# Kernel tuning notes

Hardware: AMD Instinct MI355X
Metric: run time of the kernel (lower is better)

Reference implementation:

```python
import jax, jax.numpy as jnp
import numpy as np

L, D, H, FF = 6, 768, 12, 3072
DH = D // H
EPS = 1e-12

def _layer_norm(x, g, b):
    mu = jnp.mean(x, axis=-1, keepdims=True)
    var = jnp.mean((x - mu) ** 2, axis=-1, keepdims=True)
    return (x - mu) * jax.lax.rsqrt(var + EPS) * g + b

def setup_inputs() -> dict:
    key = jax.random.key(0)
    ks = jax.random.split(key, 12)
    s = 0.02
    inp = {
        "x": jax.random.normal(ks[0], (8, 512, D), dtype=jnp.float32),
        "attn_mask": jnp.ones((8, 512), dtype=jnp.int32),
        "Wq": jax.random.normal(ks[1], (L, D, D), dtype=jnp.float32) * s,
        "bq": jnp.zeros((L, D), dtype=jnp.float32),
        "Wk": jax.random.normal(ks[2], (L, D, D), dtype=jnp.float32) * s,
        "bk": jnp.zeros((L, D), dtype=jnp.float32),
        "Wv": jax.random.normal(ks[3], (L, D, D), dtype=jnp.float32) * s,
        "bv": jnp.zeros((L, D), dtype=jnp.float32),
        "Wo": jax.random.normal(ks[4], (L, D, D), dtype=jnp.float32) * s,
        "bo": jnp.zeros((L, D), dtype=jnp.float32),
        "ln1_g": jnp.ones((L, D), dtype=jnp.float32),
        "ln1_b": jnp.zeros((L, D), dtype=jnp.float32),
        "W1": jax.random.normal(ks[5], (L, D, FF), dtype=jnp.float32) * s,
        "b1": jnp.zeros((L, FF), dtype=jnp.float32),
        "W2": jax.random.normal(ks[6], (L, FF, D), dtype=jnp.float32) * s,
        "b2": jnp.zeros((L, D), dtype=jnp.float32),
        "ln2_g": jnp.ones((L, D), dtype=jnp.float32),
        "ln2_b": jnp.zeros((L, D), dtype=jnp.float32),
    }
    return inp

def reference(x, attn_mask, Wq, bq, Wk, bk, Wv, bv, Wo, bo,
              ln1_g, ln1_b, W1, b1, W2, b2, ln2_g, ln2_b):
    bs, S, _ = x.shape
    mask_neg = (attn_mask == 0)[:, None, None, :]  # (bs,1,1,S)
    h = x
    for i in range(L):
        def split_heads(t):
            return t.reshape(bs, S, H, DH).transpose(0, 2, 1, 3)  # (bs,H,S,dh)
        q = split_heads(h @ Wq[i] + bq[i]) / jnp.sqrt(jnp.float32(DH))
        k = split_heads(h @ Wk[i] + bk[i])
        v = split_heads(h @ Wv[i] + bv[i])
        scores = jnp.einsum('bhqd,bhkd->bhqk', q, k)
        scores = jnp.where(mask_neg, jnp.float32(-1e9), scores)
        w = jax.nn.softmax(scores, axis=-1)
        ctx = jnp.einsum('bhqk,bhkd->bhqd', w, v)
        ctx = ctx.transpose(0, 2, 1, 3).reshape(bs, S, D)
        sa = ctx @ Wo[i] + bo[i]
        h2 = _layer_norm(sa + h, ln1_g[i], ln1_b[i])
        ffn = jax.nn.gelu(h2 @ W1[i] + b1[i], approximate=False) @ W2[i] + b2[i]
        h = _layer_norm(ffn + h2, ln2_g[i], ln2_b[i])
    return h
```

## Files before the change

kernel.cpp:

```cpp
#include <hip/hip_runtime.h>
#include <math.h>

#define NLAYER 6
#define DMODEL 768
#define NHEAD 12
#define DHEAD 64
#define FFDIM 3072
#define SEQ 512
#define BATCH 8
#define NTOK (BATCH * SEQ)
#define ND ((size_t)NTOK * DMODEL)

typedef __bf16 bf16_t;
typedef __bf16 bf16x8 __attribute__((ext_vector_type(8)));
typedef float f32x4 __attribute__((ext_vector_type(4)));

__device__ __forceinline__ float bf2f(ushort u) {
    return __uint_as_float(((unsigned int)u) << 16);
}
union BFU { __bf16 h; ushort u; };
__device__ __forceinline__ ushort f2b(float x) { BFU c; c.h = (__bf16)x; return c.u; }

#define GLDS(gp, lp) __builtin_amdgcn_global_load_lds( \
    (const __attribute__((address_space(1))) void*)(gp), \
    (__attribute__((address_space(3))) void*)(lp), 16, 0, 0)

__global__ __launch_bounds__(256) void gemm_mfma(
    const ushort* __restrict__ A, const ushort* __restrict__ Bt,
    const float* __restrict__ bias, float* __restrict__ Cf,
    ushort* __restrict__ Cb, int M, int K, int N, int act)
{
    __shared__ __align__(16) ushort As[8192];
    __shared__ __align__(16) ushort Bs[8192];

    const int t = threadIdx.x;
    const int w = t >> 6, l = t & 63;
    const int wr = w >> 1, wc = w & 1;
    const int row0 = blockIdx.y * 128, col0 = blockIdx.x * 128;

    f32x4 acc[4][4];
#pragma unroll
    for (int mi = 0; mi < 4; ++mi)
#pragma unroll
        for (int ni = 0; ni < 4; ++ni)
#pragma unroll
            for (int e = 0; e < 4; ++e) acc[mi][ni][e] = 0.f;

    const int c0 = t,       r0 = c0 >> 2, kg0 = (c0 & 3) ^ ((r0 >> 1) & 3);
    const int c1 = t + 256, r1 = c1 >> 2, kg1 = (c1 & 3) ^ ((r1 >> 1) & 3);
    const ushort* gA0 = A + (size_t)(row0 + r0) * K + kg0 * 8;
    const ushort* gA1 = A + (size_t)(row0 + r1) * K + kg1 * 8;
    const ushort* gB0 = Bt + (size_t)(col0 + r0) * K + kg0 * 8;
    const ushort* gB1 = Bt + (size_t)(col0 + r1) * K + kg1 * 8;

    const int lm = l & 15, lq = l >> 4;
    int aoff[4], boff[4];
#pragma unroll
    for (int mi = 0; mi < 4; ++mi) {
        int m = wr * 64 + mi * 16 + lm;
        aoff[mi] = m * 32 + (lq ^ ((m >> 1) & 3)) * 8;
    }
#pragma unroll
    for (int ni = 0; ni < 4; ++ni) {
        int n = wc * 64 + ni * 16 + lm;
        boff[ni] = n * 32 + (lq ^ ((n >> 1) & 3)) * 8;
    }

#define STAGE_FF(b, k0) do {                                  \
        GLDS(gA0 + (k0), &As[(b) * 4096 + w * 512]);          \
        GLDS(gA1 + (k0), &As[(b) * 4096 + 2048 + w * 512]);   \
        GLDS(gB0 + (k0), &Bs[(b) * 4096 + w * 512]);          \
        GLDS(gB1 + (k0), &Bs[(b) * 4096 + 2048 + w * 512]);   \
    } while (0)

#define COMPUTE_FF(b) do {                                                  \
        bf16x8 af[4], bfr[4];                                               \
        _Pragma("unroll")                                                   \
        for (int mi = 0; mi < 4; ++mi)                                      \
            af[mi] = *(const bf16x8*)&As[(b) * 4096 + aoff[mi]];            \
        _Pragma("unroll")                                                   \
        for (int ni = 0; ni < 4; ++ni)                                      \
            bfr[ni] = *(const bf16x8*)&Bs[(b) * 4096 + boff[ni]];           \
        _Pragma("unroll")                                                   \
        for (int mi = 0; mi < 4; ++mi)                                      \
            _Pragma("unroll")                                               \
            for (int ni = 0; ni < 4; ++ni)                                  \
                acc[mi][ni] = __builtin_amdgcn_mfma_f32_16x16x32_bf16(      \
                    af[mi], bfr[ni], acc[mi][ni], 0, 0, 0);                 \
    } while (0)

    const int nsteps = K >> 5;
    STAGE_FF(0, 0);
    __syncthreads();
    int cur = 0;
    for (int s = 0; s < nsteps - 1; ++s) {
        STAGE_FF(cur ^ 1, (s + 1) * 32);
        COMPUTE_FF(cur);
        __syncthreads();
        cur ^= 1;
    }
    COMPUTE_FF(cur);

#pragma unroll
    for (int mi = 0; mi < 4; ++mi) {
        int rowb = row0 + wr * 64 + mi * 16 + lq * 4;
#pragma unroll
        for (int ni = 0; ni < 4; ++ni) {
            int col = col0 + wc * 64 + ni * 16 + lm;
            float bv = bias[col];
#pragma unroll
            for (int r = 0; r < 4; ++r) {
                float v = acc[mi][ni][r] + bv;
                if (act == 1) v = 0.5f * v * (1.0f + erff(v * 0.70710678118654752f));
                size_t idx = (size_t)(rowb + r) * N + col;
                if (Cb) ((bf16_t*)Cb)[idx] = (bf16_t)v;
                else    Cf[idx] = v;
            }
        }
    }
#undef STAGE_FF
#undef COMPUTE_FF
}

__global__ __launch_bounds__(256) void gemm_mfma_sk(
    const ushort* __restrict__ A, const ushort* __restrict__ Bt,
    const float* __restrict__ bias, float* __restrict__ P0,
    float* __restrict__ P1, int M, int K, int N, int kLen)
{
    __shared__ __align__(16) ushort As[4096];
    __shared__ __align__(16) ushort Bs[8192];

    const int t = threadIdx.x;
    const int w = t >> 6, l = t & 63;
    const int wr = w >> 1, wc = w & 1;
    const int row0 = blockIdx.y * 64, col0 = blockIdx.x * 128;
    const int z = blockIdx.z;
    const int kOff = z * kLen;
    float* Pz = (z == 0) ? P0 : P1;

    f32x4 acc[2][4];
#pragma unroll
    for (int mi = 0; mi < 2; ++mi)
#pragma unroll
        for (int ni = 0; ni < 4; ++ni)
#pragma unroll
            for (int e = 0; e < 4; ++e) acc[mi][ni][e] = 0.f;

    const int rS = t >> 2, kg = (t & 3) ^ ((rS >> 1) & 3);
    const ushort* gA  = A  + (size_t)(row0 + rS) * K + kg * 8;
    const ushort* gB0 = Bt + (size_t)(col0 + rS) * K + kg * 8;
    const ushort* gB1 = Bt + (size_t)(col0 + 64 + rS) * K + kg * 8;

    const int lm = l & 15, lq = l >> 4;
    int aoff[2], boff[4];
#pragma unroll
    for (int mi = 0; mi < 2; ++mi) {
        int m = wr * 32 + mi * 16 + lm;
        aoff[mi] = m * 32 + (lq ^ ((m >> 1) & 3)) * 8;
    }
#pragma unroll
    for (int ni = 0; ni < 4; ++ni) {
        int n = wc * 64 + ni * 16 + lm;
        boff[ni] = n * 32 + (lq ^ ((n >> 1) & 3)) * 8;
    }

#define STAGE_SK(b, k0) do {                                  \
        GLDS(gA  + (k0), &As[(b) * 2048 + w * 512]);          \
        GLDS(gB0 + (k0), &Bs[(b) * 4096 + w * 512]);          \
        GLDS(gB1 + (k0), &Bs[(b) * 4096 + 2048 + w * 512]);   \
    } while (0)

#define COMPUTE_SK(b) do {                                                  \
        bf16x8 af[2], bfr[4];                                               \
        _Pragma("unroll")                                                   \
        for (int mi = 0; mi < 2; ++mi)                                      \
            af[mi] = *(const bf16x8*)&As[(b) * 2048 + aoff[mi]];            \
        _Pragma("unroll")                                                   \
        for (int ni = 0; ni < 4; ++ni)                                      \
            bfr[ni] = *(const bf16x8*)&Bs[(b) * 4096 + boff[ni]];           \
        _Pragma("unroll")                                                   \
        for (int mi = 0; mi < 2; ++mi)                                      \
            _Pragma("unroll")                                               \
            for (int ni = 0; ni < 4; ++ni)                                  \
                acc[mi][ni] = __builtin_amdgcn_mfma_f32_16x16x32_bf16(      \
                    af[mi], bfr[ni], acc[mi][ni], 0, 0, 0);                 \
    } while (0)

    const int nsteps = kLen >> 5;
    STAGE_SK(0, kOff);
    __syncthreads();
    int cur = 0;
    for (int s = 0; s < nsteps - 1; ++s) {
        STAGE_SK(cur ^ 1, kOff + (s + 1) * 32);
        COMPUTE_SK(cur);
        __syncthreads();
        cur ^= 1;
    }
    COMPUTE_SK(cur);

#pragma unroll
    for (int mi = 0; mi < 2; ++mi) {
        int rowb = row0 + wr * 32 + mi * 16 + lq * 4;
#pragma unroll
        for (int ni = 0; ni < 4; ++ni) {
            int col = col0 + wc * 64 + ni * 16 + lm;
            float bv = (z == 0) ? bias[col] : 0.f;
#pragma unroll
            for (int r = 0; r < 4; ++r)
                Pz[(size_t)(rowb + r) * N + col] = acc[mi][ni][r] + bv;
        }
    }
#undef STAGE_SK
#undef COMPUTE_SK
}

__global__ __launch_bounds__(256) void gemm_qkv(
    const ushort* __restrict__ A, const ushort* __restrict__ Bt,
    const float* __restrict__ bq, const float* __restrict__ bk,
    const float* __restrict__ bv,
    ushort* __restrict__ qb, ushort* __restrict__ kb, ushort* __restrict__ vtb)
{
    __shared__ __align__(16) ushort As[4096];
    __shared__ __align__(16) ushort Bs[8192];

    const int K = DMODEL;
    const int t = threadIdx.x;
    const int w = t >> 6, l = t & 63;
    const int wr = w >> 1, wc = w & 1;
    const int row0 = blockIdx.y * 64, col0 = blockIdx.x * 128;
    const int seg = blockIdx.x / 6;

    f32x4 acc[2][4];
#pragma unroll
    for (int mi = 0; mi < 2; ++mi)
#pragma unroll
        for (int ni = 0; ni < 4; ++ni)
#pragma unroll
            for (int e = 0; e < 4; ++e) acc[mi][ni][e] = 0.f;

    const int rS = t >> 2, kg = (t & 3) ^ ((rS >> 1) & 3);
    const ushort* gA  = A  + (size_t)(row0 + rS) * K + kg * 8;
    const ushort* gB0 = Bt + (size_t)(col0 + rS) * K + kg * 8;
    const ushort* gB1 = Bt + (size_t)(col0 + 64 + rS) * K + kg * 8;

    const int lm = l & 15, lq = l >> 4;
    int aoff[2], boff[4];
#pragma unroll
    for (int mi = 0; mi < 2; ++mi) {
        int m = wr * 32 + mi * 16 + lm;
        aoff[mi] = m * 32 + (lq ^ ((m >> 1) & 3)) * 8;
    }
#pragma unroll
    for (int ni = 0; ni < 4; ++ni) {
        int n = wc * 64 + ni * 16 + lm;
        boff[ni] = n * 32 + (lq ^ ((n >> 1) & 3)) * 8;
    }

#define STAGE_QKV(b, k0) do {                                 \
        GLDS(gA  + (k0), &As[(b) * 2048 + w * 512]);          \
        GLDS(gB0 + (k0), &Bs[(b) * 4096 + w * 512]);          \
        GLDS(gB1 + (k0), &Bs[(b) * 4096 + 2048 + w * 512]);   \
    } while (0)

#define COMPUTE_QKV(b) do {                                                 \
        bf16x8 af[2], bfr[4];                                               \
        _Pragma("unroll")                                                   \
        for (int mi = 0; mi < 2; ++mi)                                      \
            af[mi] = *(const bf16x8*)&As[(b) * 2048 + aoff[mi]];            \
        _Pragma("unroll")                                                   \
        for (int ni = 0; ni < 4; ++ni)                                      \
            bfr[ni] = *(const bf16x8*)&Bs[(b) * 4096 + boff[ni]];           \
        _Pragma("unroll")                                                   \
        for (int mi = 0; mi < 2; ++mi)                                      \
            _Pragma("unroll")                                               \
            for (int ni = 0; ni < 4; ++ni)                                  \
                acc[mi][ni] = __builtin_amdgcn_mfma_f32_16x16x32_bf16(      \
                    af[mi], bfr[ni], acc[mi][ni], 0, 0, 0);                 \
    } while (0)

    const int nsteps = K >> 5;
    STAGE_QKV(0, 0);
    __syncthreads();
    int cur = 0;
    for (int s = 0; s < nsteps - 1; ++s) {
        STAGE_QKV(cur ^ 1, (s + 1) * 32);
        COMPUTE_QKV(cur);
        __syncthreads();
        cur ^= 1;
    }
    COMPUTE_QKV(cur);

    const float* bp = (seg == 0) ? bq : (seg == 1) ? bk : bv;
    const float sc = (seg == 0) ? 0.125f : 1.0f;
#pragma unroll
    for (int mi = 0; mi < 2; ++mi) {
        int rowb = row0 + wr * 32 + mi * 16 + lq * 4;
#pragma unroll
        for (int ni = 0; ni < 4; ++ni) {
            int col = col0 + wc * 64 + ni * 16 + lm;
            int lcol = col - seg * 768;
            float bvv = bp[lcol];
            if (seg == 2) {
                int hh = lcol >> 6, dd = lcol & 63;
                int bb = rowb >> 9, ss = rowb & 511;
                ushort4 o;
                o.x = f2b(acc[mi][ni][0] + bvv);
                o.y = f2b(acc[mi][ni][1] + bvv);
                o.z = f2b(acc[mi][ni][2] + bvv);
                o.w = f2b(acc[mi][ni][3] + bvv);
                *(ushort4*)&vtb[(((size_t)(bb * NHEAD + hh)) * DHEAD + dd) * SEQ + ss] = o;
            } else {
                ushort* dst = seg ? kb : qb;
#pragma unroll
                for (int r = 0; r < 4; ++r)
                    dst[(size_t)(rowb + r) * DMODEL + lcol] = f2b((acc[mi][ni][r] + bvv) * sc);
            }
        }
    }
#undef STAGE_QKV
#undef COMPUTE_QKV
}

#define QSTR 72

__global__ __launch_bounds__(256) void attn_mfma(
    const ushort* __restrict__ qb, const ushort* __restrict__ kb,
    const ushort* __restrict__ vtb, const int* __restrict__ mask,
    ushort* __restrict__ ctxb)
{
    __shared__ __align__(16) ushort Qs[64 * QSTR];
    __shared__ __align__(16) ushort Ks[64 * QSTR];
    __shared__ __align__(16) ushort Vs[64 * QSTR];
    __shared__ __align__(16) ushort Ps[64 * QSTR];
    __shared__ float Ma[64];

    const int qt = blockIdx.x, h = blockIdx.y, b = blockIdx.z;
    const int t = threadIdx.x;
    const int w = t >> 6, l = t & 63;
    const int lm = l & 15, lq = l >> 4;

#pragma unroll
    for (int i = 0; i < 2; ++i) {
        int ch = t + i * 256;
        int r = ch >> 3, c8 = ch & 7;
        *(uint4*)&Qs[r * QSTR + c8 * 8] =
            *(const uint4*)&qb[((size_t)(b * SEQ + qt * 64 + r)) * DMODEL + h * DHEAD + c8 * 8];
    }

    f32x4 O[4];
#pragma unroll
    for (int n0 = 0; n0 < 4; ++n0)
#pragma unroll
        for (int e = 0; e < 4; ++e) O[n0][e] = 0.f;
    float mrow[4] = {-3.4e38f, -3.4e38f, -3.4e38f, -3.4e38f};
    float lrow[4] = {0.f, 0.f, 0.f, 0.f};

    const int qrow = w * 16 + lm;
    const int prow = w * 16 + lq * 4;

    for (int kt = 0; kt < SEQ / 64; ++kt) {
#pragma unroll
        for (int i = 0; i < 2; ++i) {
            int ch = t + i * 256;
            int r = ch >> 3, c8 = ch & 7;
            *(uint4*)&Ks[r * QSTR + c8 * 8] =
                *(const uint4*)&kb[((size_t)(b * SEQ + kt * 64 + r)) * DMODEL + h * DHEAD + c8 * 8];
            *(uint4*)&Vs[r * QSTR + c8 * 8] =
                *(const uint4*)&vtb[(((size_t)(b * NHEAD + h)) * DHEAD + r) * SEQ + kt * 64 + c8 * 8];
        }
        if (t < 64) Ma[t] = (mask[b * SEQ + kt * 64 + t] == 0) ? -1e9f : 0.f;
        __syncthreads();

        bf16x8 aq0 = *(const bf16x8*)&Qs[qrow * QSTR + lq * 8];
        bf16x8 aq1 = *(const bf16x8*)&Qs[qrow * QSTR + lq * 8 + 32];
        f32x4 S[4];
#pragma unroll
        for (int n0 = 0; n0 < 4; ++n0) {
#pragma unroll
            for (int e = 0; e < 4; ++e) S[n0][e] = 0.f;
            bf16x8 b0 = *(const bf16x8*)&Ks[(n0 * 16 + lm) * QSTR + lq * 8];
            bf16x8 b1 = *(const bf16x8*)&Ks[(n0 * 16 + lm) * QSTR + lq * 8 + 32];
            S[n0] = __builtin_amdgcn_mfma_f32_16x16x32_bf16(aq0, b0, S[n0], 0, 0, 0);
            S[n0] = __builtin_amdgcn_mfma_f32_16x16x32_bf16(aq1, b1, S[n0], 0, 0, 0);
        }

        float ma4[4];
#pragma unroll
        for (int n0 = 0; n0 < 4; ++n0) ma4[n0] = Ma[n0 * 16 + lm];
#pragma unroll
        for (int n0 = 0; n0 < 4; ++n0)
#pragma unroll
            for (int r = 0; r < 4; ++r) S[n0][r] += ma4[n0];

        float tm[4];
#pragma unroll
        for (int r = 0; r < 4; ++r)
            tm[r] = fmaxf(fmaxf(S[0][r], S[1][r]), fmaxf(S[2][r], S[3][r]));
#pragma unroll
        for (int off = 1; off < 16; off <<= 1)
#pragma unroll
            for (int r = 0; r < 4; ++r)
                tm[r] = fmaxf(tm[r], __shfl_xor(tm[r], off, 64));

        float al[4], ts[4];
#pragma unroll
        for (int r = 0; r < 4; ++r) {
            float mn = fmaxf(mrow[r], tm[r]);
            al[r] = __expf(mrow[r] - mn);
            mrow[r] = mn;
            ts[r] = 0.f;
        }
#pragma unroll
        for (int n0 = 0; n0 < 4; ++n0)
#pragma unroll
            for (int r = 0; r < 4; ++r) {
                float p = __expf(S[n0][r] - mrow[r]);
                ts[r] += p;
                Ps[(prow + r) * QSTR + n0 * 16 + lm] = f2b(p);
            }
#pragma unroll
        for (int off = 1; off < 16; off <<= 1)
#pragma unroll
            for (int r = 0; r < 4; ++r)
                ts[r] += __shfl_xor(ts[r], off, 64);
#pragma unroll
        for (int r = 0; r < 4; ++r) lrow[r] = lrow[r] * al[r] + ts[r];
#pragma unroll
        for (int n0 = 0; n0 < 4; ++n0)
#pragma unroll
            for (int r = 0; r < 4; ++r) O[n0][r] *= al[r];

        bf16x8 ap0 = *(const bf16x8*)&Ps[qrow * QSTR + lq * 8];
        bf16x8 ap1 = *(const bf16x8*)&Ps[qrow * QSTR + lq * 8 + 32];
#pragma unroll
        for (int n0 = 0; n0 < 4; ++n0) {
            bf16x8 v0 = *(const bf16x8*)&Vs[(n0 * 16 + lm) * QSTR + lq * 8];
            bf16x8 v1 = *(const bf16x8*)&Vs[(n0 * 16 + lm) * QSTR + lq * 8 + 32];
            O[n0] = __builtin_amdgcn_mfma_f32_16x16x32_bf16(ap0, v0, O[n0], 0, 0, 0);
            O[n0] = __builtin_amdgcn_mfma_f32_16x16x32_bf16(ap1, v1, O[n0], 0, 0, 0);
        }
        __syncthreads();
    }

    float inv[4];
#pragma unroll
    for (int r = 0; r < 4; ++r) inv[r] = 1.f / lrow[r];
#pragma unroll
    for (int n0 = 0; n0 < 4; ++n0)
#pragma unroll
        for (int r = 0; r < 4; ++r)
            Ks[(prow + r) * QSTR + n0 * 16 + lm] = f2b(O[n0][r] * inv[r]);
    __syncthreads();
#pragma unroll
    for (int i = 0; i < 2; ++i) {
        int ch = t + i * 256;
        int r = ch >> 3, c8 = ch & 7;
        *(uint4*)&ctxb[((size_t)(b * SEQ + qt * 64 + r)) * DMODEL + h * DHEAD + c8 * 8] =
            *(const uint4*)&Ks[r * QSTR + c8 * 8];
    }
}

__global__ __launch_bounds__(256) void transpose_w(
    const float* __restrict__ Wq, const float* __restrict__ Wk,
    const float* __restrict__ Wv, const float* __restrict__ Wo,
    const float* __restrict__ W1, const float* __restrict__ W2,
    ushort* __restrict__ Wqt, ushort* __restrict__ Wkt,
    ushort* __restrict__ Wvt, ushort* __restrict__ Wot,
    ushort* __restrict__ W1t, ushort* __restrict__ W2t)
{
    __shared__ float tile[32][33];
    const int bid = blockIdx.x;
    const float* src; ushort* dst; int K, N, tx, ty;
    if (bid < 2304) {
        int m = bid / 576, tl = bid % 576;
        src = (m == 0) ? Wq : (m == 1) ? Wk : (m == 2) ? Wv : Wo;
        dst = (m == 0) ? Wqt : (m == 1) ? Wkt : (m == 2) ? Wvt : Wot;
        K = 768; N = 768; tx = tl % 24; ty = tl / 24;
    } else if (bid < 4608) {
        int tl = bid - 2304;
        src = W1; dst = W1t; K = 768; N = 3072; tx = tl % 96; ty = tl / 96;
    } else {
        int tl = bid - 4608;
        src = W2; dst = W2t; K = 3072; N = 768; tx = tl % 24; ty = tl / 24;
    }
    const int t = threadIdx.x;
    const int lx = t & 31, ly = t >> 5;
    const int n0 = tx * 32, k0 = ty * 32;
#pragma unroll
    for (int i = 0; i < 4; ++i)
        tile[lx][ly + i * 8] = src[(size_t)(k0 + ly + i * 8) * N + n0 + lx];
    __syncthreads();
#pragma unroll
    for (int i = 0; i < 4; ++i)
        ((bf16_t*)dst)[(size_t)(n0 + ly + i * 8) * K + k0 + lx] =
            (bf16_t)tile[ly + i * 8][lx];
}

__global__ __launch_bounds__(256) void f2bf_kernel(
    const float* __restrict__ src, ushort* __restrict__ dst)
{
    const size_t i = ((size_t)blockIdx.x * 256 + threadIdx.x) * 4;
    float4 v = *(const float4*)(src + i);
    ushort4 o;
    o.x = f2b(v.x); o.y = f2b(v.y); o.z = f2b(v.z); o.w = f2b(v.w);
    *(ushort4*)(dst + i) = o;
}

__global__ __launch_bounds__(256) void add_ln3_kernel(
    const float* __restrict__ p0, const float* __restrict__ p1,
    const float* __restrict__ res,
    const float* __restrict__ gw, const float* __restrict__ bw,
    float* __restrict__ out, ushort* __restrict__ outb)
{
    const int row = blockIdx.x;
    const int t = threadIdx.x;
    __shared__ float red[8];

    const float* a0 = p0 + (size_t)row * DMODEL;
    const float* a1 = p1 + (size_t)row * DMODEL;
    const float* rr = res + (size_t)row * DMODEL;

    float vals[3];
    float s = 0.f;
#pragma unroll
    for (int i = 0; i < 3; ++i) {
        int c = t + i * 256;
        vals[i] = a0[c] + a1[c] + rr[c];
        s += vals[i];
    }
#pragma unroll
    for (int off = 32; off > 0; off >>= 1) s += __shfl_down(s, off, 64);
    if ((t & 63) == 0) red[t >> 6] = s;
    __syncthreads();
    const float mu = (red[0] + red[1] + red[2] + red[3]) * (1.0f / DMODEL);

    float vs = 0.f;
#pragma unroll
    for (int i = 0; i < 3; ++i) {
        float d = vals[i] - mu;
        vs += d * d;
    }
#pragma unroll
    for (int off = 32; off > 0; off >>= 1) vs += __shfl_down(vs, off, 64);
    if ((t & 63) == 0) red[4 + (t >> 6)] = vs;
    __syncthreads();
    const float var = (red[4] + red[5] + red[6] + red[7]) * (1.0f / DMODEL);
    const float inv = rsqrtf(var + 1e-12f);

#pragma unroll
    for (int i = 0; i < 3; ++i) {
        int c = t + i * 256;
        float v = (vals[i] - mu) * inv * gw[c] + bw[c];
        out[(size_t)row * DMODEL + c] = v;
        ((bf16_t*)outb)[(size_t)row * DMODEL + c] = (bf16_t)v;
    }
}

extern "C" void kernel_launch(void* const* d_in, const int* in_sizes, int n_in,
                              void* d_out, int out_size, void* d_ws, size_t ws_size,
                              hipStream_t stream)
{
    const float* x    = (const float*)d_in[0];
    const int*   mask = (const int*)d_in[1];
    const float* Wq = (const float*)d_in[2];
    const float* bq = (const float*)d_in[3];
    const float* Wk = (const float*)d_in[4];
    const float* bk = (const float*)d_in[5];
    const float* Wv = (const float*)d_in[6];
    const float* bv = (const float*)d_in[7];
    const float* Wo = (const float*)d_in[8];
    const float* bo = (const float*)d_in[9];
    const float* ln1g = (const float*)d_in[10];
    const float* ln1b = (const float*)d_in[11];
    const float* W1 = (const float*)d_in[12];
    const float* b1 = (const float*)d_in[13];
    const float* W2 = (const float*)d_in[14];
    const float* b2 = (const float*)d_in[15];
    const float* ln2g = (const float*)d_in[16];
    const float* ln2b = (const float*)d_in[17];

    float* f32b = (float*)d_ws;
    float* hbuf = f32b;
    float* f1   = f32b + ND;
    float* h2   = f32b + 2 * ND;
    ushort* ub  = (ushort*)(f32b + 3 * ND);
    ushort* qb  = ub;
    ushort* kb  = ub + ND;
    ushort* vtb = ub + 2 * ND;
    ushort* hb  = ub + 3 * ND;
    ushort* U   = ub + 4 * ND;
    ushort* ctxb = U;
    ushort* Wqkvt = U + (size_t)NTOK * FFDIM;
    ushort* Wot = Wqkvt + 3 * 768 * 768;
    ushort* W1t = Wot + 768 * 768;
    ushort* W2t = W1t + (size_t)768 * 3072;

    float* p1 = (float*)ub;

    hipMemcpyAsync(hbuf, x, ND * sizeof(float), hipMemcpyDeviceToDevice, stream);
    f2bf_kernel<<<(int)(ND / 1024), 256, 0, stream>>>(x, hb);

    const dim3 gQKV(18, 64);
    const dim3 gSK(6, 64, 2);
    const dim3 gFF(24, 32);
    const dim3 gA(SEQ / 64, NHEAD, BATCH);

    for (int l = 0; l < NLAYER; ++l) {
        const float* Wq_l = Wq + (size_t)l * DMODEL * DMODEL;
        const float* Wk_l = Wk + (size_t)l * DMODEL * DMODEL;
        const float* Wv_l = Wv + (size_t)l * DMODEL * DMODEL;
        const float* Wo_l = Wo + (size_t)l * DMODEL * DMODEL;
        const float* W1_l = W1 + (size_t)l * DMODEL * FFDIM;
        const float* W2_l = W2 + (size_t)l * FFDIM * DMODEL;

        transpose_w<<<6912, 256, 0, stream>>>(Wq_l, Wk_l, Wv_l, Wo_l, W1_l, W2_l,
                                              Wqkvt, Wqkvt + 768 * 768,
                                              Wqkvt + 2 * 768 * 768, Wot, W1t, W2t);

        gemm_qkv<<<gQKV, 256, 0, stream>>>(hb, Wqkvt,
                                           bq + (size_t)l * DMODEL,
                                           bk + (size_t)l * DMODEL,
                                           bv + (size_t)l * DMODEL,
                                           qb, kb, vtb);

        attn_mfma<<<gA, 256, 0, stream>>>(qb, kb, vtb, mask, ctxb);

        gemm_mfma_sk<<<gSK, 256, 0, stream>>>(ctxb, Wot, bo + (size_t)l * DMODEL,
                                              f1, p1, NTOK, DMODEL, DMODEL, DMODEL / 2);

        add_ln3_kernel<<<NTOK, 256, 0, stream>>>(f1, p1, hbuf,
                                                 ln1g + (size_t)l * DMODEL,
                                                 ln1b + (size_t)l * DMODEL, h2, hb);

        gemm_mfma<<<gFF, 256, 0, stream>>>(hb, W1t, b1 + (size_t)l * FFDIM,
                                           nullptr, U, NTOK, DMODEL, FFDIM, 1);

        gemm_mfma_sk<<<gSK, 256, 0, stream>>>(U, W2t, b2 + (size_t)l * DMODEL,
                                              f1, p1, NTOK, FFDIM, DMODEL, FFDIM / 2);

        float* hout = (l == NLAYER - 1) ? (float*)d_out : hbuf;
        add_ln3_kernel<<<NTOK, 256, 0, stream>>>(f1, p1, h2,
                                                 ln2g + (size_t)l * DMODEL,
                                                 ln2b + (size_t)l * DMODEL, hout, hb);
    }
}
```

Before: 1.284 ms.

## Swizzle GEMM workgroup order for XCDs, vectorize layernorm and transpose, fuse init

Remaps workgroup indices in all three GEMM kernels so consecutive blocks land on the same XCD (stride-8 interleave), aiming to improve L2 reuse of A/B tiles. Rewrites add+layernorm to use 192 threads with float4 loads and stores, writes the transpose output as paired bf16 stores, and merges the initial memcpy and bf16 conversion into one kernel. The swizzle assumes grid sizes divisible by 8 and hardcodes grid dimensions in two kernels.

Result: faster. 1.247 ms (-2.8%).

```diff
diff --git a/kernel.cpp b/kernel.cpp
--- a/kernel.cpp
+++ b/kernel.cpp
@@ -36,7 +36,13 @@
     const int t = threadIdx.x;
     const int w = t >> 6, l = t & 63;
     const int wr = w >> 1, wc = w & 1;
-    const int row0 = blockIdx.y * 128, col0 = blockIdx.x * 128;
+
+    const int hw = blockIdx.x + gridDim.x * blockIdx.y;
+    const int nwg = gridDim.x * gridDim.y;
+    const int sw = (hw & 7) * (nwg >> 3) + (hw >> 3);
+    const int bx = sw % gridDim.x, by = sw / gridDim.x;
+
+    const int row0 = by * 128, col0 = bx * 128;
 
     f32x4 acc[4][4];
 #pragma unroll
@@ -89,11 +95,11 @@
                     af[mi], bfr[ni], acc[mi][ni], 0, 0, 0);                 \
     } while (0)
 
-    const int nsteps = K >> 5;
+    const int nst = K >> 5;
     STAGE_FF(0, 0);
     __syncthreads();
     int cur = 0;
-    for (int s = 0; s < nsteps - 1; ++s) {
+    for (int s = 0; s < nst - 1; ++s) {
         STAGE_FF(cur ^ 1, (s + 1) * 32);
         COMPUTE_FF(cur);
         __syncthreads();
@@ -133,8 +139,14 @@
     const int t = threadIdx.x;
     const int w = t >> 6, l = t & 63;
     const int wr = w >> 1, wc = w & 1;
-    const int row0 = blockIdx.y * 64, col0 = blockIdx.x * 128;
-    const int z = blockIdx.z;
+
+    const int hw = blockIdx.x + 6 * blockIdx.y + 384 * blockIdx.z;
+    const int sw = (hw & 7) * 96 + (hw >> 3);
+    const int z  = sw / 384;
+    const int rr_ = sw - z * 384;
+    const int bx = rr_ % 6, by = rr_ / 6;
+
+    const int row0 = by * 64, col0 = bx * 128;
     const int kOff = z * kLen;
     float* Pz = (z == 0) ? P0 : P1;
 
@@ -186,11 +198,11 @@
                     af[mi], bfr[ni], acc[mi][ni], 0, 0, 0);                 \
     } while (0)
 
-    const int nsteps = kLen >> 5;
+    const int nst = kLen >> 5;
     STAGE_SK(0, kOff);
     __syncthreads();
     int cur = 0;
-    for (int s = 0; s < nsteps - 1; ++s) {
+    for (int s = 0; s < nst - 1; ++s) {
         STAGE_SK(cur ^ 1, kOff + (s + 1) * 32);
         COMPUTE_SK(cur);
         __syncthreads();
@@ -227,8 +239,13 @@
     const int t = threadIdx.x;
     const int w = t >> 6, l = t & 63;
     const int wr = w >> 1, wc = w & 1;
-    const int row0 = blockIdx.y * 64, col0 = blockIdx.x * 128;
-    const int seg = blockIdx.x / 6;
+
+    const int hw = blockIdx.x + 18 * blockIdx.y;
+    const int sw = (hw & 7) * 144 + (hw >> 3);
+    const int bx = sw % 18, by = sw / 18;
+
+    const int row0 = by * 64, col0 = bx * 128;
+    const int seg = bx / 6;
 
     f32x4 acc[2][4];
 #pragma unroll
@@ -278,11 +295,11 @@
                     af[mi], bfr[ni], acc[mi][ni], 0, 0, 0);                 \
     } while (0)
 
-    const int nsteps = K >> 5;
+    const int nst = K >> 5;
     STAGE_QKV(0, 0);
     __syncthreads();
     int cur = 0;
-    for (int s = 0; s < nsteps - 1; ++s) {
+    for (int s = 0; s < nst - 1; ++s) {
         STAGE_QKV(cur ^ 1, (s + 1) * 32);
         COMPUTE_QKV(cur);
         __syncthreads();
@@ -490,23 +507,30 @@
     for (int i = 0; i < 4; ++i)
         tile[lx][ly + i * 8] = src[(size_t)(k0 + ly + i * 8) * N + n0 + lx];
     __syncthreads();
-#pragma unroll
-    for (int i = 0; i < 4; ++i)
-        ((bf16_t*)dst)[(size_t)(n0 + ly + i * 8) * K + k0 + lx] =
-            (bf16_t)tile[ly + i * 8][lx];
-}
-
-__global__ __launch_bounds__(256) void f2bf_kernel(
-    const float* __restrict__ src, ushort* __restrict__ dst)
+    const int kk2 = (t & 15) * 2, nn = t >> 4;
+#pragma unroll
+    for (int i = 0; i < 2; ++i) {
+        int nl = nn + i * 16;
+        ushort2 o;
+        o.x = f2b(tile[nl][kk2]);
+        o.y = f2b(tile[nl][kk2 + 1]);
+        *(ushort2*)&dst[(size_t)(n0 + nl) * K + k0 + kk2] = o;
+    }
+}
+
+__global__ __launch_bounds__(256) void init_kernel(
+    const float* __restrict__ x, float* __restrict__ hbuf,
+    ushort* __restrict__ hb)
 {
     const size_t i = ((size_t)blockIdx.x * 256 + threadIdx.x) * 4;
-    float4 v = *(const float4*)(src + i);
+    float4 v = *(const float4*)(x + i);
+    *(float4*)(hbuf + i) = v;
     ushort4 o;
     o.x = f2b(v.x); o.y = f2b(v.y); o.z = f2b(v.z); o.w = f2b(v.w);
-    *(ushort4*)(dst + i) = o;
-}
-
-__global__ __launch_bounds__(256) void add_ln3_kernel(
+    *(ushort4*)(hb + i) = o;
+}
+
+__global__ __launch_bounds__(192) void add_ln3_kernel(
     const float* __restrict__ p0, const float* __restrict__ p1,
     const float* __restrict__ res,
     const float* __restrict__ gw, const float* __restrict__ bw,
@@ -514,46 +538,45 @@
 {
     const int row = blockIdx.x;
     const int t = threadIdx.x;
-    __shared__ float red[8];
-
-    const float* a0 = p0 + (size_t)row * DMODEL;
-    const float* a1 = p1 + (size_t)row * DMODEL;
-    const float* rr = res + (size_t)row * DMODEL;
-
-    float vals[3];
-    float s = 0.f;
-#pragma unroll
-    for (int i = 0; i < 3; ++i) {
-        int c = t + i * 256;
-        vals[i] = a0[c] + a1[c] + rr[c];
-        s += vals[i];
-    }
+    __shared__ float red[6];
+
+    const float4 v0 = ((const float4*)(p0 + (size_t)row * DMODEL))[t];
+    const float4 v1 = ((const float4*)(p1 + (size_t)row * DMODEL))[t];
+    const float4 v2 = ((const float4*)(res + (size_t)row * DMODEL))[t];
+
+    float4 vv;
+    vv.x = v0.x + v1.x + v2.x;
+    vv.y = v0.y + v1.y + v2.y;
+    vv.z = v0.z + v1.z + v2.z;
+    vv.w = v0.w + v1.w + v2.w;
+
+    float s = (vv.x + vv.y) + (vv.z + vv.w);
 #pragma unroll
     for (int off = 32; off > 0; off >>= 1) s += __shfl_down(s, off, 64);
     if ((t & 63) == 0) red[t >> 6] = s;
     __syncthreads();
-    const float mu = (red[0] + red[1] + red[2] + red[3]) * (1.0f / DMODEL);
-
-    float vs = 0.f;
-#pragma unroll
-    for (int i = 0; i < 3; ++i) {
-        float d = vals[i] - mu;
-        vs += d * d;
-    }
+    const float mu = (red[0] + red[1] + red[2]) * (1.0f / DMODEL);
+
+    float dx = vv.x - mu, dy = vv.y - mu, dz = vv.z - mu, dw = vv.w - mu;
+    float vs = (dx * dx + dy * dy) + (dz * dz + dw * dw);
 #pragma unroll
     for (int off = 32; off > 0; off >>= 1) vs += __shfl_down(vs, off, 64);
-    if ((t & 63) == 0) red[4 + (t >> 6)] = vs;
+    if ((t & 63) == 0) red[3 + (t >> 6)] = vs;
     __syncthreads();
-    const float var = (red[4] + red[5] + red[6] + red[7]) * (1.0f / DMODEL);
+    const float var = (red[3] + red[4] + red[5]) * (1.0f / DMODEL);
     const float inv = rsqrtf(var + 1e-12f);
 
-#pragma unroll
-    for (int i = 0; i < 3; ++i) {
-        int c = t + i * 256;
-        float v = (vals[i] - mu) * inv * gw[c] + bw[c];
-        out[(size_t)row * DMODEL + c] = v;
-        ((bf16_t*)outb)[(size_t)row * DMODEL + c] = (bf16_t)v;
-    }
+    const float4 g = ((const float4*)gw)[t];
+    const float4 bb = ((const float4*)bw)[t];
+    float4 o;
+    o.x = dx * inv * g.x + bb.x;
+    o.y = dy * inv * g.y + bb.y;
+    o.z = dz * inv * g.z + bb.z;
+    o.w = dw * inv * g.w + bb.w;
+    ((float4*)(out + (size_t)row * DMODEL))[t] = o;
+    ushort4 ob;
+    ob.x = f2b(o.x); ob.y = f2b(o.y); ob.z = f2b(o.z); ob.w = f2b(o.w);
+    ((ushort4*)(outb + (size_t)row * DMODEL * 0 + (size_t)row * DMODEL))[t] = ob;
 }
 
 extern "C" void kernel_launch(void* const* d_in, const int* in_sizes, int n_in,
@@ -597,8 +620,7 @@
 
     float* p1 = (float*)ub;
 
-    hipMemcpyAsync(hbuf, x, ND * sizeof(float), hipMemcpyDeviceToDevice, stream);
-    f2bf_kernel<<<(int)(ND / 1024), 256, 0, stream>>>(x, hb);
+    init_kernel<<<(int)(ND / 1024), 256, 0, stream>>>(x, hbuf, hb);
 
     const dim3 gQKV(18, 64);
     const dim3 gSK(6, 64, 2);
@@ -628,7 +650,7 @@
         gemm_mfma_sk<<<gSK, 256, 0, stream>>>(ctxb, Wot, bo + (size_t)l * DMODEL,
                                               f1, p1, NTOK, DMODEL, DMODEL, DMODEL / 2);
 
-        add_ln3_kernel<<<NTOK, 256, 0, stream>>>(f1, p1, hbuf,
+        add_ln3_kernel<<<NTOK, 192, 0, stream>>>(f1, p1, hbuf,
                                                  ln1g + (size_t)l * DMODEL,
                                                  ln1b + (size_t)l * DMODEL, h2, hb);
 
@@ -639,7 +661,7 @@
                                               f1, p1, NTOK, FFDIM, DMODEL, FFDIM / 2);
 
         float* hout = (l == NLAYER - 1) ? (float*)d_out : hbuf;
-        add_ln3_kernel<<<NTOK, 256, 0, stream>>>(f1, p1, h2,
+        add_ln3_kernel<<<NTOK, 192, 0, stream>>>(f1, p1, h2,
                                                  ln2g + (size_t)l * DMODEL,
                                                  ln2b + (size_t)l * DMODEL, hout, hb);
     }
```
